# Performance work log

Hardware: AMD Instinct MI355X
Metric: run time of the kernel (lower is better)

Reference implementation:

```python
import jax, jax.numpy as jnp
import numpy as np

# dims
L, E, D, DFF, H = 4, 4, 512, 2048, 8
B, T, S, K = 16, 256, 512, 2
HD = D // H


def _ln(x, g, b, eps=1e-5):
    m = x.mean(-1, keepdims=True)
    v = ((x - m) ** 2).mean(-1, keepdims=True)
    return (x - m) / jnp.sqrt(v + eps) * g + b


def _mha(xq, xkv, in_w, in_b, out_w, out_b):
    # torch nn.MultiheadAttention (batch_first), no masks, eval mode
    qw, kw, vw = jnp.split(in_w, 3, axis=0)
    qb, kb, vb = jnp.split(in_b, 3)
    q = xq @ qw.T + qb                       # [B,T,D]
    k = xkv @ kw.T + kb                      # [B,S,D]
    v = xkv @ vw.T + vb
    def heads(t):
        b, s, _ = t.shape
        return t.reshape(b, s, H, HD).transpose(0, 2, 1, 3)
    q, k, v = heads(q), heads(k), heads(v)   # [B,H,*,HD]
    scale = 1.0 / float(np.sqrt(HD))
    a = jax.nn.softmax(jnp.einsum('bhtd,bhsd->bhts', q, k) * scale, axis=-1)
    o = jnp.einsum('bhts,bhsd->bhtd', a, v)
    o = o.transpose(0, 2, 1, 3).reshape(xq.shape[0], xq.shape[1], D)
    return o @ out_w.T + out_b


def _expert(p, x, mem):
    (siw, sib, sow, sob, ciw, cib, cow, cob,
     l1w, l1b, l2w, l2b, g1, b1, g2, b2, g3, b3) = p
    sa = _mha(x, x, siw, sib, sow, sob)
    x = _ln(x + sa, g1, b1)
    ca = _mha(x, mem, ciw, cib, cow, cob)
    x = _ln(x + ca, g2, b2)
    ffn = jax.nn.relu(x @ l1w.T + l1b) @ l2w.T + l2b
    x = _ln(x + ffn, g3, b3)
    return x


def _forward(tgt, memory, router_w, params):
    x = tgt
    for l in range(L):
        pooled = x.mean(axis=1)                      # [B,D] sample-level routing
        logits = pooled @ router_w[l].T              # [B,E]
        vals, idx = jax.lax.top_k(logits, K)
        w = jax.nn.softmax(vals.astype(jnp.float32), axis=-1).astype(x.dtype)
        # dense [B,E] combine weights: zero for unselected experts -> same math
        wf = jnp.zeros((x.shape[0], E), x.dtype).at[jnp.arange(x.shape[0])[:, None], idx].add(w)
        p_l = jax.tree_util.tree_map(lambda a: a[l], params)   # each [E,...]
        outs = jax.vmap(_expert, in_axes=(0, None, None))(p_l, x, memory)  # [E,B,T,D]
        x = jnp.einsum('be,ebtd->btd', wf, outs)
    return x


def setup_inputs() -> dict:
    key = jax.random.key(0)
    ks = jax.random.split(key, 16)
    n = lambda k, shape: jax.random.normal(k, shape, jnp.float32) * 0.02
    return {
        'tgt': jax.random.normal(ks[0], (B, T, D), jnp.float32),
        'memory': jax.random.normal(ks[1], (B, S, D), jnp.float32),
        'router_w': n(ks[2], (L, E, D)),
        'sa_in_w': n(ks[3], (L, E, 3 * D, D)), 'sa_in_b': jnp.zeros((L, E, 3 * D)),
        'sa_out_w': n(ks[4], (L, E, D, D)), 'sa_out_b': jnp.zeros((L, E, D)),
        'ca_in_w': n(ks[5], (L, E, 3 * D, D)), 'ca_in_b': jnp.zeros((L, E, 3 * D)),
        'ca_out_w': n(ks[6], (L, E, D, D)), 'ca_out_b': jnp.zeros((L, E, D)),
        'lin1_w': n(ks[7], (L, E, DFF, D)), 'lin1_b': jnp.zeros((L, E, DFF)),
        'lin2_w': n(ks[8], (L, E, D, DFF)), 'lin2_b': jnp.zeros((L, E, D)),
        'n1_g': jnp.ones((L, E, D)), 'n1_b': jnp.zeros((L, E, D)),
        'n2_g': jnp.ones((L, E, D)), 'n2_b': jnp.zeros((L, E, D)),
        'n3_g': jnp.ones((L, E, D)), 'n3_b': jnp.zeros((L, E, D)),
    }


def reference(tgt, memory, router_w, sa_in_w, sa_in_b, sa_out_w, sa_out_b,
              ca_in_w, ca_in_b, ca_out_w, ca_out_b, lin1_w, lin1_b, lin2_w, lin2_b,
              n1_g, n1_b, n2_g, n2_b, n3_g, n3_b):
    params = (sa_in_w, sa_in_b, sa_out_w, sa_out_b, ca_in_w, ca_in_b, ca_out_w, ca_out_b,
              lin1_w, lin1_b, lin2_w, lin2_b, n1_g, n1_b, n2_g, n2_b, n3_g, n3_b)
    return _forward(tgt, memory, router_w, params)
```

## Files before the change

kernel.cpp:

```cpp
#include <hip/hip_runtime.h>
#include <hip/hip_bf16.h>

#define L_ 4
#define E_ 4
#define D_ 512
#define DFF_ 2048
#define H_ 8
#define B_ 16
#define T_ 256
#define S_ 512
#define HD_ 64
#define NSLOT 32

typedef __attribute__((ext_vector_type(4))) float f32x4;
typedef __attribute__((ext_vector_type(8))) short bf16x8;
typedef __attribute__((ext_vector_type(4))) int i32x4;

static __device__ __forceinline__ float bf2f(unsigned short u){
  union{float f; unsigned u;} c; c.u = ((unsigned)u)<<16; return c.f;
}
static __device__ __forceinline__ unsigned short f2bf(float f){
  union{float f; unsigned u;} c; c.f=f;
  unsigned u=c.u;
  return (unsigned short)((u + 0x7FFFu + ((u>>16)&1u))>>16);
}

static __device__ __forceinline__ void gload16(const unsigned short* g, unsigned short* l){
  __builtin_amdgcn_global_load_lds(
      (const __attribute__((address_space(1))) void*)g,
      (__attribute__((address_space(3))) void*)l, 16, 0, 0);
}

static __device__ __forceinline__ int xcd_swz(int orig, int nwg){
  int q = nwg >> 3, r = nwg & 7;
  int xcd = orig & 7, idx = orig >> 3;
  return (xcd < r) ? (xcd*(q+1) + idx) : (r*(q+1) + (xcd-r)*q + idx);
}

__global__ void __launch_bounds__(256) pool_k(const float* __restrict__ x,
    float* __restrict__ part)
{
  int b = blockIdx.x >> 3, ch = blockIdx.x & 7;
  int tid = threadIdx.x;
  const float* xp = x + ((long)b*T_ + ch*32)*D_ + tid*2;
  float s0=0.f, s1=0.f;
  #pragma unroll 8
  for (int t=0;t<32;t++){
    float2 v = *(const float2*)(xp + (long)t*D_);
    s0 += v.x; s1 += v.y;
  }
  float* pp = part + ((long)b*8 + ch)*D_ + tid*2;
  pp[0]=s0; pp[1]=s1;
}

__global__ void __launch_bounds__(256) route2_k(const float* __restrict__ part,
    const float* __restrict__ rw, int* __restrict__ eidx, float* __restrict__ wgt)
{
  __shared__ float pooled[D_];
  __shared__ float logit[E_];
  int b = blockIdx.x, tid = threadIdx.x;
  for (int d = tid; d < D_; d += 256){
    float s = 0.f;
    #pragma unroll
    for (int c=0;c<8;c++) s += part[((long)b*8 + c)*D_ + d];
    pooled[d] = s * (1.f/T_);
  }
  __syncthreads();
  int wave = tid>>6, lane = tid&63;
  {
    float s=0.f;
    const float* w = rw + (long)wave*D_;
    for (int d=lane; d<D_; d+=64) s += pooled[d]*w[d];
    #pragma unroll
    for (int o=32;o;o>>=1) s += __shfl_xor(s,o);
    if (lane==0) logit[wave] = s;
  }
  __syncthreads();
  if (tid==0){
    int i1=0; float v1=logit[0];
    for (int e=1;e<E_;e++) if (logit[e] > v1){ v1=logit[e]; i1=e; }
    int i2=-1; float v2=-3.4e38f;
    for (int e=0;e<E_;e++) if (e!=i1 && logit[e] > v2){ v2=logit[e]; i2=e; }
    float e2 = __expf(v2 - v1);
    float w1 = 1.f/(1.f+e2);
    eidx[2*b]=i1; eidx[2*b+1]=i2;
    wgt[2*b]=w1; wgt[2*b+1]=e2*w1;
  }
}

__global__ void __launch_bounds__(256) cast_bf16_k(const float* __restrict__ in,
    unsigned short* __restrict__ out, long n){
  long i = ((long)blockIdx.x*blockDim.x + threadIdx.x)*4;
  long st = (long)gridDim.x*blockDim.x*4;
  for (; i<n; i+=st){
    float4 v = *(const float4*)(in+i);
    ushort4 o; o.x=f2bf(v.x); o.y=f2bf(v.y); o.z=f2bf(v.z); o.w=f2bf(v.w);
    *(ushort4*)(out+i) = o;
  }
}

__global__ void __launch_bounds__(256) cast_weights_k(
    const float* __restrict__ s0, const float* __restrict__ s1,
    const float* __restrict__ s2, const float* __restrict__ s3,
    const float* __restrict__ s4, const float* __restrict__ s5,
    unsigned short* __restrict__ d0, unsigned short* __restrict__ d1,
    unsigned short* __restrict__ d2, unsigned short* __restrict__ d3,
    unsigned short* __restrict__ d4, unsigned short* __restrict__ d5)
{
  const long N0=(long)E_*3*D_*D_, N1=(long)E_*D_*D_;
  const long N2=N0, N3=N1, N4=(long)E_*DFF_*D_, N5=N4;
  const long total = N0+N1+N2+N3+N4+N5;
  long i = ((long)blockIdx.x*256 + threadIdx.x)*4;
  long st = (long)gridDim.x*256*4;
  for (; i<total; i+=st){
    const float* s; unsigned short* d; long j = i;
    if (j < N0){ s=s0; d=d0; }
    else if ((j-=N0) < N1){ s=s1; d=d1; }
    else if ((j-=N1) < N2){ s=s2; d=d2; }
    else if ((j-=N2) < N3){ s=s3; d=d3; }
    else if ((j-=N3) < N4){ s=s4; d=d4; }
    else { j-=N4; s=s5; d=d5; }
    float4 v = *(const float4*)(s+j);
    ushort4 o; o.x=f2bf(v.x); o.y=f2bf(v.y); o.z=f2bf(v.z); o.w=f2bf(v.w);
    *(ushort4*)(d+j) = o;
  }
}

__global__ void __launch_bounds__(256) vtrans_k(const unsigned short* __restrict__ src,
    long sSlot, int ld, unsigned short* __restrict__ dst, int rows)
{
  __shared__ unsigned short t[64][68];
  int s0 = blockIdx.x*64; int h = blockIdx.y; int slot = blockIdx.z;
  const unsigned short* sp = src + (long)slot*sSlot + (long)h*64;
  int c = threadIdx.x&63, w = threadIdx.x>>6;
  #pragma unroll
  for (int i=0;i<16;i++){
    int r = i*4 + w;
    t[r][c] = sp[(long)(s0+r)*ld + c];
  }
  __syncthreads();
  unsigned short* dp = dst + ((long)slot*H_ + h)*((long)64*rows) + s0;
  #pragma unroll
  for (int i=0;i<16;i++){
    int d = i*4 + w;
    dp[(long)d*rows + c] = t[c][d];
  }
}

template<int NT>
__global__ void __launch_bounds__(512) fattn_k(
    const unsigned short* __restrict__ Qg, long qSlot, int ldq,
    const unsigned short* __restrict__ Kg, long kSlot, int ldk,
    const unsigned short* __restrict__ Vtg,
    unsigned short* __restrict__ Og, long oSlot, int ldo)
{
  constexpr int SLEN = NT*64;
  __shared__ unsigned short K_lds[64][72];
  __shared__ unsigned short V_lds[64][72];
  __shared__ unsigned short P_lds[8][16][72];

  int nwg = gridDim.x*gridDim.y;
  int wg = xcd_swz(blockIdx.x + gridDim.x*blockIdx.y, nwg);
  int qb = wg % gridDim.x;
  int z  = wg / gridDim.x;
  int slot = z >> 3, h = z & 7;
  int tid = threadIdx.x, wave = tid>>6, lane = tid&63;
  int lr = lane&15, lg = lane>>4;
  int lk = lg*8;

  const unsigned short* Qp = Qg + (long)slot*qSlot + (long)h*HD_;
  const unsigned short* Kp = Kg + (long)slot*kSlot + (long)h*HD_;
  const unsigned short* Vp = Vtg + (long)z*((long)HD_*SLEN);

  bf16x8 qf[2];
  {
    int qrow = qb*128 + wave*16 + lr;
    const unsigned short* qr = Qp + (long)qrow*ldq;
    qf[0] = *(const bf16x8*)(qr + lk);
    qf[1] = *(const bf16x8*)(qr + 32 + lk);
  }

  float m_prev[4], l_run[4];
  f32x4 acc_o[4];
  #pragma unroll
  for (int r=0;r<4;r++){ m_prev[r]=-1e30f; l_run[r]=0.f; }
  #pragma unroll
  for (int ni=0;ni<4;ni++) acc_o[ni]=(f32x4){0.f,0.f,0.f,0.f};

  int srow = tid>>3, sch = tid&7;

  i32x4 kr0 = *(const i32x4*)(Kp + (long)srow*ldk + sch*8);
  i32x4 vr0 = *(const i32x4*)(Vp + (long)srow*SLEN + sch*8);

  for (int t=0; t<NT; ++t){
    __syncthreads();
    *(i32x4*)&K_lds[srow][sch*8] = kr0;
    *(i32x4*)&V_lds[srow][sch*8] = vr0;
    __syncthreads();

    int tn = (t+1 < NT) ? t+1 : t;
    int k0n = tn*64;
    kr0 = *(const i32x4*)(Kp + (long)(k0n+srow)*ldk + sch*8);
    vr0 = *(const i32x4*)(Vp + (long)srow*SLEN + k0n + sch*8);

    f32x4 s[4];
    #pragma unroll
    for (int ni=0;ni<4;ni++) s[ni]=(f32x4){0.f,0.f,0.f,0.f};
    __builtin_amdgcn_s_setprio(1);
    #pragma unroll
    for (int ki=0;ki<2;ki++){
      #pragma unroll
      for (int ni=0;ni<4;ni++){
        bf16x8 kf = *(const bf16x8*)&K_lds[ni*16+lr][ki*32+lk];
        s[ni] = __builtin_amdgcn_mfma_f32_16x16x32_bf16(qf[ki], kf, s[ni],0,0,0);
      }
    }
    __builtin_amdgcn_s_setprio(0);
    float tmax[4];
    #pragma unroll
    for (int r=0;r<4;r++){
      tmax[r] = fmaxf(fmaxf(s[0][r],s[1][r]),fmaxf(s[2][r],s[3][r]));
      #pragma unroll
      for (int msk=1; msk<16; msk<<=1) tmax[r]=fmaxf(tmax[r], __shfl_xor(tmax[r],msk));
    }
    bool inc = (tmax[0]>m_prev[0])|(tmax[1]>m_prev[1])|(tmax[2]>m_prev[2])|(tmax[3]>m_prev[3]);
    if (__any(inc)){
      #pragma unroll
      for (int r=0;r<4;r++){
        float mnew = fmaxf(m_prev[r], tmax[r]);
        float corr = __expf(m_prev[r]-mnew);
        m_prev[r] = mnew;
        l_run[r] *= corr;
        #pragma unroll
        for (int ni=0;ni<4;ni++) acc_o[ni][r] *= corr;
      }
    }
    float rs[4] = {0.f,0.f,0.f,0.f};
    #pragma unroll
    for (int ni=0;ni<4;ni++){
      #pragma unroll
      for (int r=0;r<4;r++){
        float p = __expf(s[ni][r]-m_prev[r]);
        rs[r] += p;
        P_lds[wave][lg*4+r][ni*16+lr] = f2bf(p);
      }
    }
    #pragma unroll
    for (int r=0;r<4;r++){
      #pragma unroll
      for (int msk=1; msk<16; msk<<=1) rs[r] += __shfl_xor(rs[r],msk);
      l_run[r] += rs[r];
    }
    __builtin_amdgcn_s_setprio(1);
    #pragma unroll
    for (int ki=0;ki<2;ki++){
      bf16x8 pf = *(const bf16x8*)&P_lds[wave][lr][ki*32+lk];
      #pragma unroll
      for (int ni=0;ni<4;ni++){
        bf16x8 vf = *(const bf16x8*)&V_lds[ni*16+lr][ki*32+lk];
        acc_o[ni] = __builtin_amdgcn_mfma_f32_16x16x32_bf16(pf, vf, acc_o[ni],0,0,0);
      }
    }
    __builtin_amdgcn_s_setprio(0);
  }
  unsigned short* Op = Og + (long)slot*oSlot + (long)h*HD_;
  #pragma unroll
  for (int r=0;r<4;r++){
    float inv = 1.f/l_run[r];
    int q = qb*128 + wave*16 + lg*4 + r;
    #pragma unroll
    for (int ni=0;ni<4;ni++)
      Op[(long)q*ldo + ni*16 + lr] = f2bf(acc_o[ni][r]*inv);
  }
}

template<int BM, int BN, int WTM, int WTN, int BK>
__global__ void __launch_bounds__(512) gemm_lds(
    const unsigned short* __restrict__ A, long aSlot, int aDiv, long aHead, int lda,
    const unsigned short* __restrict__ W, long wSlot, long wHead, long wExp, int ldw,
    const int* __restrict__ eidx, const float* __restrict__ bias, long biasExp,
    void* __restrict__ Cp, long cSlot, long cHead, int ldc,
    int K, int HZ, int f32out, int relu, int scaleNlim, float scaleVal)
{
  constexpr int WAVES_N = BN/WTN;
  constexpr int MI = WTM/16, NI = WTN/16;
  constexpr int SLOTS = BK/8;
  static_assert((BM/WTM)*(BN/WTN) == 8, "8 waves");
  static_assert((BM*SLOTS)%512==0 && (BN*SLOTS)%512==0, "stage coverage");
  __shared__ unsigned short smem[2*(BM+BN)*BK];

  int nwg = gridDim.x*gridDim.y*gridDim.z;
  int wg = xcd_swz(blockIdx.x + gridDim.x*(blockIdx.y + gridDim.y*blockIdx.z), nwg);
  int bx = wg % gridDim.x; int t1 = wg / gridDim.x;
  int by = t1 % gridDim.y; int z  = t1 / gridDim.y;

  int slot = z / HZ;
  int h = z - slot*HZ;
  int e = eidx ? eidx[slot] : 0;
  const unsigned short* Ap = A + (long)(slot/aDiv)*aSlot + (long)h*aHead;
  const unsigned short* Wp = W + (long)slot*wSlot + (long)h*wHead + (long)e*wExp;
  const float* bp = bias ? (bias + (long)e*biasExp) : nullptr;

  int tid  = threadIdx.x;
  int wave = tid>>6, lane = tid&63;
  int wm = wave / WAVES_N, wn = wave % WAVES_N;
  int bm0 = by*BM;
  int bn0 = bx*BN;
  int lr = lane&15;
  int lg = lane>>4;
  int swz = (BK==64) ? (lr&7) : ((lr>>1)&3);

  Ap += (long)bm0*lda;
  Wp += (long)bn0*ldw;

  f32x4 acc[MI][NI];
  #pragma unroll
  for (int i=0;i<MI;i++)
  #pragma unroll
  for (int j=0;j<NI;j++) acc[i][j] = (f32x4){0.f,0.f,0.f,0.f};

  auto stage = [&](int buf, int k0){
    unsigned short* as = &smem[(size_t)buf*(BM+BN)*BK];
    unsigned short* bs = as + BM*BK;
    #pragma unroll
    for (int i=0;i<BM*SLOTS/512;i++){
      int cch = i*512 + tid;
      int row = cch / SLOTS, c = cch % SLOTS;
      int cs = (BK==64) ? (c ^ (row&7)) : (c ^ ((row>>1)&3));
      gload16(Ap + (long)row*lda + k0 + (cs<<3), as + cch*8);
    }
    #pragma unroll
    for (int i=0;i<BN*SLOTS/512;i++){
      int cch = i*512 + tid;
      int row = cch / SLOTS, c = cch % SLOTS;
      int cs = (BK==64) ? (c ^ (row&7)) : (c ^ ((row>>1)&3));
      gload16(Wp + (long)row*ldw + k0 + (cs<<3), bs + cch*8);
    }
  };

  auto compute = [&](int buf){
    unsigned short* as = &smem[(size_t)buf*(BM+BN)*BK];
    unsigned short* bs = as + BM*BK;
    #pragma unroll
    for (int ki=0;ki<BK/32;ki++){
      bf16x8 af[MI], bfr[NI];
      #pragma unroll
      for (int mi=0;mi<MI;mi++){
        int row = wm*WTM + mi*16 + lr;
        af[mi] = *(const bf16x8*)&as[row*BK + (((ki*4+lg) ^ swz)<<3)];
      }
      #pragma unroll
      for (int ni=0;ni<NI;ni++){
        int row = wn*WTN + ni*16 + lr;
        bfr[ni] = *(const bf16x8*)&bs[row*BK + (((ki*4+lg) ^ swz)<<3)];
      }
      __builtin_amdgcn_s_setprio(1);
      #pragma unroll
      for (int mi=0;mi<MI;mi++)
      #pragma unroll
      for (int ni=0;ni<NI;ni++)
        acc[mi][ni] = __builtin_amdgcn_mfma_f32_16x16x32_bf16(af[mi], bfr[ni], acc[mi][ni], 0,0,0);
      __builtin_amdgcn_s_setprio(0);
    }
  };

  int NT = K / BK;
  stage(0, 0);
  __syncthreads();
  int cur = 0;
  for (int t=0; t<NT; ++t){
    if (t+1 < NT) stage(cur^1, (t+1)*BK);
    compute(cur);
    __syncthreads();
    cur ^= 1;
  }

  long cbase = (long)slot*cSlot + (long)h*cHead;
  int rbase = lg*4;
  #pragma unroll
  for (int mi=0;mi<MI;mi++)
  #pragma unroll
  for (int ni=0;ni<NI;ni++){
    f32x4 v = acc[mi][ni];
    int n = bn0 + wn*WTN + ni*16 + lr;
    float bv = bp ? bp[n] : 0.f;
    float scv = (n < scaleNlim) ? scaleVal : 1.f;
    #pragma unroll
    for (int r=0;r<4;r++){
      int m = bm0 + wm*WTM + mi*16 + rbase + r;
      float val = (v[r] + bv) * scv;
      if (relu) val = fmaxf(val, 0.f);
      long o = cbase + (long)m*ldc + n;
      if (f32out) ((float*)Cp)[o] = val;
      else ((unsigned short*)Cp)[o] = f2bf(val);
    }
  }
}

template<int ABF>
__global__ void __launch_bounds__(256) add_ln_k(
    const void* __restrict__ Ab_, int aDiv, long aStride,
    const unsigned short* __restrict__ Bb, long bStride,
    const float* __restrict__ G, const float* __restrict__ Bt,
    const int* __restrict__ eidx,
    unsigned short* __restrict__ OutB)
{
  int row = blockIdx.x*4 + (threadIdx.x>>6);
  int slot = row>>8, t = row&255;
  int lane = threadIdx.x&63;
  int d0 = lane*8;
  float x[8];
  if (ABF){
    const unsigned short* a = (const unsigned short*)Ab_ + (long)(slot/aDiv)*aStride + (long)t*D_ + d0;
    ushort4 a0 = *(const ushort4*)a, a1 = *(const ushort4*)(a+4);
    x[0]=bf2f(a0.x); x[1]=bf2f(a0.y); x[2]=bf2f(a0.z); x[3]=bf2f(a0.w);
    x[4]=bf2f(a1.x); x[5]=bf2f(a1.y); x[6]=bf2f(a1.z); x[7]=bf2f(a1.w);
  } else {
    const float* a = (const float*)Ab_ + (long)(slot/aDiv)*aStride + (long)t*D_ + d0;
    float4 a0 = *(const float4*)a, a1 = *(const float4*)(a+4);
    x[0]=a0.x; x[1]=a0.y; x[2]=a0.z; x[3]=a0.w;
    x[4]=a1.x; x[5]=a1.y; x[6]=a1.z; x[7]=a1.w;
  }
  const unsigned short* b = Bb + (long)slot*bStride + (long)t*D_ + d0;
  ushort4 b0 = *(const ushort4*)b, b1 = *(const ushort4*)(b+4);
  x[0]+=bf2f(b0.x); x[1]+=bf2f(b0.y); x[2]+=bf2f(b0.z); x[3]+=bf2f(b0.w);
  x[4]+=bf2f(b1.x); x[5]+=bf2f(b1.y); x[6]+=bf2f(b1.z); x[7]+=bf2f(b1.w);
  float s=0.f;
  #pragma unroll
  for (int i=0;i<8;i++) s += x[i];
  #pragma unroll
  for (int o=32;o;o>>=1) s += __shfl_xor(s,o);
  float m = s*(1.f/D_);
  float q=0.f;
  #pragma unroll
  for (int i=0;i<8;i++){ float d=x[i]-m; q+=d*d; }
  #pragma unroll
  for (int o=32;o;o>>=1) q += __shfl_xor(q,o);
  float rs = rsqrtf(q*(1.f/D_)+1e-5f);
  int e = eidx[slot];
  const float* g  = G  + (long)e*D_ + d0;
  const float* bt = Bt + (long)e*D_ + d0;
  float4 g0 = *(const float4*)g, g1 = *(const float4*)(g+4);
  float4 t0 = *(const float4*)bt, t1 = *(const float4*)(bt+4);
  float gg[8] = {g0.x,g0.y,g0.z,g0.w,g1.x,g1.y,g1.z,g1.w};
  float tt[8] = {t0.x,t0.y,t0.z,t0.w,t1.x,t1.y,t1.z,t1.w};
  long ob = (long)slot*(T_*D_) + (long)t*D_ + d0;
  ushort4 o0, o1;
  float y0=(x[0]-m)*rs*gg[0]+tt[0], y1=(x[1]-m)*rs*gg[1]+tt[1];
  float y2=(x[2]-m)*rs*gg[2]+tt[2], y3=(x[3]-m)*rs*gg[3]+tt[3];
  float y4=(x[4]-m)*rs*gg[4]+tt[4], y5=(x[5]-m)*rs*gg[5]+tt[5];
  float y6=(x[6]-m)*rs*gg[6]+tt[6], y7=(x[7]-m)*rs*gg[7]+tt[7];
  o0.x=f2bf(y0); o0.y=f2bf(y1); o0.z=f2bf(y2); o0.w=f2bf(y3);
  o1.x=f2bf(y4); o1.y=f2bf(y5); o1.z=f2bf(y6); o1.w=f2bf(y7);
  *(ushort4*)(OutB+ob) = o0;
  *(ushort4*)(OutB+ob+4) = o1;
}

__global__ void __launch_bounds__(256) add_ln_comb_k(
    const unsigned short* __restrict__ x2b, const unsigned short* __restrict__ proj,
    const float* __restrict__ G, const float* __restrict__ Bt,
    const int* __restrict__ eidx, const float* __restrict__ wgt,
    float* __restrict__ dstF, unsigned short* __restrict__ dstB)
{
  int row = blockIdx.x*4 + (threadIdx.x>>6);
  int b = row>>8, t = row&255;
  int lane = threadIdx.x&63;
  int d0 = lane*8;
  float out[8];
  #pragma unroll
  for (int i=0;i<8;i++) out[i]=0.f;
  #pragma unroll
  for (int s2i=0;s2i<2;s2i++){
    int slot = 2*b + s2i;
    int e = eidx[slot];
    float w = wgt[slot];
    const unsigned short* a = x2b + (long)slot*(T_*D_) + (long)t*D_ + d0;
    const unsigned short* p = proj + (long)slot*(T_*D_) + (long)t*D_ + d0;
    ushort4 a0 = *(const ushort4*)a, a1 = *(const ushort4*)(a+4);
    ushort4 p0 = *(const ushort4*)p, p1 = *(const ushort4*)(p+4);
    float x[8];
    x[0]=bf2f(a0.x)+bf2f(p0.x); x[1]=bf2f(a0.y)+bf2f(p0.y);
    x[2]=bf2f(a0.z)+bf2f(p0.z); x[3]=bf2f(a0.w)+bf2f(p0.w);
    x[4]=bf2f(a1.x)+bf2f(p1.x); x[5]=bf2f(a1.y)+bf2f(p1.y);
    x[6]=bf2f(a1.z)+bf2f(p1.z); x[7]=bf2f(a1.w)+bf2f(p1.w);
    float s=0.f;
    #pragma unroll
    for (int i=0;i<8;i++) s += x[i];
    #pragma unroll
    for (int o=32;o;o>>=1) s += __shfl_xor(s,o);
    float m = s*(1.f/D_);
    float q=0.f;
    #pragma unroll
    for (int i=0;i<8;i++){ float d=x[i]-m; q+=d*d; }
    #pragma unroll
    for (int o=32;o;o>>=1) q += __shfl_xor(q,o);
    float rs = rsqrtf(q*(1.f/D_)+1e-5f);
    const float* g  = G  + (long)e*D_ + d0;
    const float* bt = Bt + (long)e*D_ + d0;
    float4 g0 = *(const float4*)g, g1 = *(const float4*)(g+4);
    float4 t0 = *(const float4*)bt, t1 = *(const float4*)(bt+4);
    float gg[8] = {g0.x,g0.y,g0.z,g0.w,g1.x,g1.y,g1.z,g1.w};
    float tt[8] = {t0.x,t0.y,t0.z,t0.w,t1.x,t1.y,t1.z,t1.w};
    #pragma unroll
    for (int i=0;i<8;i++) out[i] += w*((x[i]-m)*rs*gg[i]+tt[i]);
  }
  long ob = (long)row*D_ + d0;
  float4 f0 = {out[0],out[1],out[2],out[3]};
  float4 f1 = {out[4],out[5],out[6],out[7]};
  *(float4*)(dstF+ob) = f0;
  *(float4*)(dstF+ob+4) = f1;
  ushort4 o0, o1;
  o0.x=f2bf(out[0]); o0.y=f2bf(out[1]); o0.z=f2bf(out[2]); o0.w=f2bf(out[3]);
  o1.x=f2bf(out[4]); o1.y=f2bf(out[5]); o1.z=f2bf(out[6]); o1.w=f2bf(out[7]);
  *(ushort4*)(dstB+ob) = o0;
  *(ushort4*)(dstB+ob+4) = o1;
}

extern "C" void kernel_launch(void* const* d_in, const int* in_sizes, int n_in,
                              void* d_out, int out_size, void* d_ws, size_t ws_size,
                              hipStream_t stream)
{
  const float* tgt      = (const float*)d_in[0];
  const float* memory   = (const float*)d_in[1];
  const float* router_w = (const float*)d_in[2];
  const float* sa_in_w  = (const float*)d_in[3];
  const float* sa_in_b  = (const float*)d_in[4];
  const float* sa_out_w = (const float*)d_in[5];
  const float* sa_out_b = (const float*)d_in[6];
  const float* ca_in_w  = (const float*)d_in[7];
  const float* ca_in_b  = (const float*)d_in[8];
  const float* ca_out_w = (const float*)d_in[9];
  const float* ca_out_b = (const float*)d_in[10];
  const float* lin1_w   = (const float*)d_in[11];
  const float* lin1_b   = (const float*)d_in[12];
  const float* lin2_w   = (const float*)d_in[13];
  const float* lin2_b   = (const float*)d_in[14];
  const float* n1_g = (const float*)d_in[15];
  const float* n1_b = (const float*)d_in[16];
  const float* n2_g = (const float*)d_in[17];
  const float* n2_b = (const float*)d_in[18];
  const float* n3_g = (const float*)d_in[19];
  const float* n3_b = (const float*)d_in[20];

  char* ws = (char*)d_ws;
  size_t off = 0;
  auto alloc = [&](size_t bytes)->char*{
    char* p = ws + off; off += (bytes + 255) & ~(size_t)255; return p;
  };
  unsigned short* xb    = (unsigned short*)alloc(2ull*B_*T_*D_);
  unsigned short* memb  = (unsigned short*)alloc(2ull*B_*S_*D_);
  float*          x     = (float*)alloc(4ull*B_*T_*D_);
  float*          part  = (float*)alloc(4ull*B_*8*D_);
  int*            eidx  = (int*)alloc(4ull*NSLOT);
  float*          wgt   = (float*)alloc(4ull*NSLOT);
  unsigned short* wSaIn  = (unsigned short*)alloc(2ull*E_*3*D_*D_);
  unsigned short* wSaOut = (unsigned short*)alloc(2ull*E_*D_*D_);
  unsigned short* wCaIn  = (unsigned short*)alloc(2ull*E_*3*D_*D_);
  unsigned short* wCaOut = (unsigned short*)alloc(2ull*E_*D_*D_);
  unsigned short* wL1    = (unsigned short*)alloc(2ull*E_*DFF_*D_);
  unsigned short* wL2    = (unsigned short*)alloc(2ull*E_*D_*DFF_);
  unsigned short* qkv   = (unsigned short*)alloc(2ull*NSLOT*T_*3*D_);
  unsigned short* ffh   = (unsigned short*)alloc(2ull*NSLOT*T_*DFF_);
  unsigned short* attn  = (unsigned short*)alloc(2ull*NSLOT*T_*D_);
  unsigned short* proj  = (unsigned short*)alloc(2ull*NSLOT*T_*D_);
  unsigned short* x1b   = (unsigned short*)alloc(2ull*NSLOT*T_*D_);
  unsigned short* cq    = (unsigned short*)alloc(2ull*NSLOT*T_*D_);
  unsigned short* mkv   = (unsigned short*)alloc(2ull*NSLOT*S_*2*D_);
  unsigned short* x2b   = (unsigned short*)alloc(2ull*NSLOT*T_*D_);
  unsigned short* Vt1   = cq;
  unsigned short* Vt2   = qkv;

  cast_bf16_k<<<1024,256,0,stream>>>(tgt,    xb,   (long)B_*T_*D_);
  cast_bf16_k<<<1024,256,0,stream>>>(memory, memb, (long)B_*S_*D_);

  const float* xcur = tgt;
  for (int l=0; l<L_; ++l){
    pool_k<<<B_*8,256,0,stream>>>(xcur, part);
    route2_k<<<B_,256,0,stream>>>(part, router_w + (size_t)l*E_*D_, eidx, wgt);
    cast_weights_k<<<2048,256,0,stream>>>(
      sa_in_w  + (size_t)l*E_*3*D_*D_, sa_out_w + (size_t)l*E_*D_*D_,
      ca_in_w  + (size_t)l*E_*3*D_*D_, ca_out_w + (size_t)l*E_*D_*D_,
      lin1_w   + (size_t)l*E_*DFF_*D_, lin2_w   + (size_t)l*E_*D_*DFF_,
      wSaIn, wSaOut, wCaIn, wCaOut, wL1, wL2);

    gemm_lds<128,256,64,64,32><<<dim3(6,2,NSLOT),512,0,stream>>>(
      xb, (long)T_*D_, 2, 0, D_,
      wSaIn, 0, 0, (long)3*D_*D_, D_,
      eidx, sa_in_b + (size_t)l*E_*3*D_, 3*D_,
      qkv, (long)T_*3*D_, 0, 3*D_,
      512, 1, 0, 0, D_, 0.125f);
    vtrans_k<<<dim3(T_/64,H_,NSLOT),256,0,stream>>>(
      qkv + 2*D_, (long)T_*3*D_, 3*D_, Vt1, T_);
    fattn_k<4><<<dim3(T_/128, NSLOT*H_),512,0,stream>>>(
      qkv, (long)T_*3*D_, 3*D_,
      qkv + D_, (long)T_*3*D_, 3*D_,
      Vt1, attn, (long)T_*D_, D_);
    gemm_lds<64,128,32,32,64><<<dim3(4,4,NSLOT),512,0,stream>>>(
      attn, (long)T_*D_, 1, 0, D_,
      wSaOut, 0, 0, (long)D_*D_, D_,
      eidx, sa_out_b + (size_t)l*E_*D_, D_,
      proj, (long)T_*D_, 0, D_,
      512, 1, 0, 0, 0, 1.f);
    add_ln_k<0><<<2048,256,0,stream>>>(xcur, 2, (long)T_*D_, proj, (long)T_*D_,
      n1_g + (size_t)l*E_*D_, n1_b + (size_t)l*E_*D_, eidx, x1b);
    gemm_lds<64,128,32,32,64><<<dim3(4,4,NSLOT),512,0,stream>>>(
      x1b, (long)T_*D_, 1, 0, D_,
      wCaIn, 0, 0, (long)3*D_*D_, D_,
      eidx, ca_in_b + (size_t)l*E_*3*D_, 3*D_,
      cq, (long)T_*D_, 0, D_,
      512, 1, 0, 0, D_, 0.125f);
    gemm_lds<128,256,64,64,32><<<dim3(4,4,NSLOT),512,0,stream>>>(
      memb, (long)S_*D_, 2, 0, D_,
      wCaIn + (size_t)D_*D_, 0, 0, (long)3*D_*D_, D_,
      eidx, ca_in_b + (size_t)l*E_*3*D_ + D_, 3*D_,
      mkv, (long)S_*2*D_, 0, 2*D_,
      512, 1, 0, 0, 0, 1.f);
    vtrans_k<<<dim3(S_/64,H_,NSLOT),256,0,stream>>>(
      mkv + D_, (long)S_*2*D_, 2*D_, Vt2, S_);
    fattn_k<8><<<dim3(T_/128, NSLOT*H_),512,0,stream>>>(
      cq, (long)T_*D_, D_,
      mkv, (long)S_*2*D_, 2*D_,
      Vt2, attn, (long)T_*D_, D_);
    gemm_lds<64,128,32,32,64><<<dim3(4,4,NSLOT),512,0,stream>>>(
      attn, (long)T_*D_, 1, 0, D_,
      wCaOut, 0, 0, (long)D_*D_, D_,
      eidx, ca_out_b + (size_t)l*E_*D_, D_,
      proj, (long)T_*D_, 0, D_,
      512, 1, 0, 0, 0, 1.f);
    add_ln_k<1><<<2048,256,0,stream>>>(x1b, 1, (long)T_*D_, proj, (long)T_*D_,
      n2_g + (size_t)l*E_*D_, n2_b + (size_t)l*E_*D_, eidx, x2b);
    gemm_lds<128,256,64,64,32><<<dim3(8,2,NSLOT),512,0,stream>>>(
      x2b, (long)T_*D_, 1, 0, D_,
      wL1, 0, 0, (long)DFF_*D_, D_,
      eidx, lin1_b + (size_t)l*E_*DFF_, DFF_,
      ffh, (long)T_*DFF_, 0, DFF_,
      512, 1, 0, 1, 0, 1.f);
    gemm_lds<64,128,32,32,64><<<dim3(4,4,NSLOT),512,0,stream>>>(
      ffh, (long)T_*DFF_, 1, 0, DFF_,
      wL2, 0, 0, (long)D_*DFF_, DFF_,
      eidx, lin2_b + (size_t)l*E_*D_, D_,
      proj, (long)T_*D_, 0, D_,
      2048, 1, 0, 0, 0, 1.f);
    float* dstF = (l==L_-1) ? (float*)d_out : x;
    add_ln_comb_k<<<1024,256,0,stream>>>(x2b, proj,
      n3_g + (size_t)l*E_*D_, n3_b + (size_t)l*E_*D_, eidx, wgt, dstF, xb);
    xcur = x;
  }
}
```

Measured before the change: 951.2 us.

## Merge self-attn QKV and memory KV projections into one dual GEMM launch

Moves the cross-attention memory K/V projection, which depends only on memory and routing, ahead of self-attention and fuses it with the self-attention QKV projection into a single grouped GEMM launch. The two V-transpose kernels are likewise merged into one launch, which needs a separate Vt2 buffer so the memory V transpose no longer aliases qkv. The aim is fewer kernel launches and larger grids that fill the GPU better. The cost is an extra buffer allocation and more branching in the merged kernels.

```diff
diff --git a/kernel.cpp b/kernel.cpp
--- a/kernel.cpp
+++ b/kernel.cpp
@@ -126,11 +126,18 @@
   }
 }
 
-__global__ void __launch_bounds__(256) vtrans_k(const unsigned short* __restrict__ src,
-    long sSlot, int ld, unsigned short* __restrict__ dst, int rows)
+__global__ void __launch_bounds__(256) vtrans2_k(
+    const unsigned short* __restrict__ src0, long sSlot0, int ld0,
+    unsigned short* __restrict__ dst0, int rows0,
+    const unsigned short* __restrict__ src1, long sSlot1, int ld1,
+    unsigned short* __restrict__ dst1, int rows1)
 {
   __shared__ unsigned short t[64][68];
-  int s0 = blockIdx.x*64; int h = blockIdx.y; int slot = blockIdx.z;
+  int xb = blockIdx.x;
+  const unsigned short* src; long sSlot; int ld; unsigned short* dst; int rows; int s0;
+  if (xb < rows0/64){ src=src0; sSlot=sSlot0; ld=ld0; dst=dst0; rows=rows0; s0=xb*64; }
+  else              { src=src1; sSlot=sSlot1; ld=ld1; dst=dst1; rows=rows1; s0=(xb-rows0/64)*64; }
+  int h = blockIdx.y; int slot = blockIdx.z;
   const unsigned short* sp = src + (long)slot*sSlot + (long)h*64;
   int c = threadIdx.x&63, w = threadIdx.x>>6;
   #pragma unroll
@@ -275,43 +282,24 @@
 }
 
 template<int BM, int BN, int WTM, int WTN, int BK>
-__global__ void __launch_bounds__(512) gemm_lds(
-    const unsigned short* __restrict__ A, long aSlot, int aDiv, long aHead, int lda,
-    const unsigned short* __restrict__ W, long wSlot, long wHead, long wExp, int ldw,
-    const int* __restrict__ eidx, const float* __restrict__ bias, long biasExp,
-    void* __restrict__ Cp, long cSlot, long cHead, int ldc,
-    int K, int HZ, int f32out, int relu, int scaleNlim, float scaleVal)
+static __device__ __forceinline__ void gemm_core(
+    const unsigned short* __restrict__ Ap,
+    const unsigned short* __restrict__ Wp,
+    const float* __restrict__ bp,
+    void* __restrict__ Cp, long cbase, int ldc,
+    int lda, int ldw, int bm0, int bn0,
+    int K, int f32out, int relu, int scaleNlim, float scaleVal,
+    unsigned short* smem)
 {
   constexpr int WAVES_N = BN/WTN;
   constexpr int MI = WTM/16, NI = WTN/16;
   constexpr int SLOTS = BK/8;
-  static_assert((BM/WTM)*(BN/WTN) == 8, "8 waves");
-  static_assert((BM*SLOTS)%512==0 && (BN*SLOTS)%512==0, "stage coverage");
-  __shared__ unsigned short smem[2*(BM+BN)*BK];
-
-  int nwg = gridDim.x*gridDim.y*gridDim.z;
-  int wg = xcd_swz(blockIdx.x + gridDim.x*(blockIdx.y + gridDim.y*blockIdx.z), nwg);
-  int bx = wg % gridDim.x; int t1 = wg / gridDim.x;
-  int by = t1 % gridDim.y; int z  = t1 / gridDim.y;
-
-  int slot = z / HZ;
-  int h = z - slot*HZ;
-  int e = eidx ? eidx[slot] : 0;
-  const unsigned short* Ap = A + (long)(slot/aDiv)*aSlot + (long)h*aHead;
-  const unsigned short* Wp = W + (long)slot*wSlot + (long)h*wHead + (long)e*wExp;
-  const float* bp = bias ? (bias + (long)e*biasExp) : nullptr;
-
   int tid  = threadIdx.x;
   int wave = tid>>6, lane = tid&63;
   int wm = wave / WAVES_N, wn = wave % WAVES_N;
-  int bm0 = by*BM;
-  int bn0 = bx*BN;
   int lr = lane&15;
   int lg = lane>>4;
   int swz = (BK==64) ? (lr&7) : ((lr>>1)&3);
-
-  Ap += (long)bm0*lda;
-  Wp += (long)bn0*ldw;
 
   f32x4 acc[MI][NI];
   #pragma unroll
@@ -375,7 +363,6 @@
     cur ^= 1;
   }
 
-  long cbase = (long)slot*cSlot + (long)h*cHead;
   int rbase = lg*4;
   #pragma unroll
   for (int mi=0;mi<MI;mi++)
@@ -395,6 +382,77 @@
       else ((unsigned short*)Cp)[o] = f2bf(val);
     }
   }
+}
+
+template<int BM, int BN, int WTM, int WTN, int BK>
+__global__ void __launch_bounds__(512) gemm_lds(
+    const unsigned short* __restrict__ A, long aSlot, int aDiv, long aHead, int lda,
+    const unsigned short* __restrict__ W, long wSlot, long wHead, long wExp, int ldw,
+    const int* __restrict__ eidx, const float* __restrict__ bias, long biasExp,
+    void* __restrict__ Cp, long cSlot, long cHead, int ldc,
+    int K, int HZ, int f32out, int relu, int scaleNlim, float scaleVal)
+{
+  constexpr int SLOTS = BK/8;
+  static_assert((BM/WTM)*(BN/WTN) == 8, "8 waves");
+  static_assert((BM*SLOTS)%512==0 && (BN*SLOTS)%512==0, "stage coverage");
+  __shared__ unsigned short smem[2*(BM+BN)*BK];
+
+  int nwg = gridDim.x*gridDim.y*gridDim.z;
+  int wg = xcd_swz(blockIdx.x + gridDim.x*(blockIdx.y + gridDim.y*blockIdx.z), nwg);
+  int bx = wg % gridDim.x; int t1 = wg / gridDim.x;
+  int by = t1 % gridDim.y; int z  = t1 / gridDim.y;
+
+  int slot = z / HZ;
+  int h = z - slot*HZ;
+  int e = eidx ? eidx[slot] : 0;
+  const unsigned short* Ap = A + (long)(slot/aDiv)*aSlot + (long)h*aHead + (long)by*BM*lda;
+  const unsigned short* Wp = W + (long)slot*wSlot + (long)h*wHead + (long)e*wExp + (long)bx*BN*ldw;
+  const float* bp = bias ? (bias + (long)e*biasExp) : nullptr;
+  long cbase = (long)slot*cSlot + (long)h*cHead;
+
+  gemm_core<BM,BN,WTM,WTN,BK>(Ap, Wp, bp, Cp, cbase, ldc, lda, ldw,
+      by*BM, bx*BN, K, f32out, relu, scaleNlim, scaleVal, smem);
+}
+
+__global__ void __launch_bounds__(512) gemm_dual(
+    const unsigned short* __restrict__ A0, long aSlot0,
+    const unsigned short* __restrict__ W0, const float* __restrict__ bias0,
+    unsigned short* __restrict__ C0, long cSlot0, int ldc0,
+    const unsigned short* __restrict__ A1, long aSlot1,
+    const unsigned short* __restrict__ W1, const float* __restrict__ bias1,
+    unsigned short* __restrict__ C1, long cSlot1, int ldc1,
+    const int* __restrict__ eidx)
+{
+  constexpr int BM=128, BN=256, WTM=64, WTN=64, BK=32;
+  __shared__ unsigned short smem[2*(BM+BN)*BK];
+  const int NBLK0 = 6*2*NSLOT;
+  int nwg = gridDim.x;
+  int wg = xcd_swz(blockIdx.x, nwg);
+
+  const unsigned short *Ap, *Wp; const float* bp;
+  unsigned short* Cp; long cbase; int ldc, bm0, bn0, scaleNlim;
+  if (wg < NBLK0){
+    int bx = wg % 6; int t1 = wg / 6;
+    int by = t1 % 2; int slot = t1 / 2;
+    int e = eidx[slot];
+    bm0 = by*BM; bn0 = bx*BN;
+    Ap = A0 + (long)(slot/2)*aSlot0 + (long)bm0*D_;
+    Wp = W0 + (long)e*(3*D_*D_) + (long)bn0*D_;
+    bp = bias0 + (long)e*(3*D_);
+    Cp = C0; cbase = (long)slot*cSlot0; ldc = ldc0; scaleNlim = D_;
+  } else {
+    int w1 = wg - NBLK0;
+    int bx = w1 % 4; int t1 = w1 / 4;
+    int by = t1 % 4; int slot = t1 / 4;
+    int e = eidx[slot];
+    bm0 = by*BM; bn0 = bx*BN;
+    Ap = A1 + (long)(slot/2)*aSlot1 + (long)bm0*D_;
+    Wp = W1 + (long)e*(3*D_*D_) + (long)bn0*D_;
+    bp = bias1 + (long)e*(3*D_);
+    Cp = C1; cbase = (long)slot*cSlot1; ldc = ldc1; scaleNlim = 0;
+  }
+  gemm_core<BM,BN,WTM,WTN,BK>(Ap, Wp, bp, Cp, cbase, ldc, D_, D_,
+      bm0, bn0, 512, 0, 0, scaleNlim, 0.125f, smem);
 }
 
 template<int ABF>
@@ -567,8 +625,8 @@
   unsigned short* cq    = (unsigned short*)alloc(2ull*NSLOT*T_*D_);
   unsigned short* mkv   = (unsigned short*)alloc(2ull*NSLOT*S_*2*D_);
   unsigned short* x2b   = (unsigned short*)alloc(2ull*NSLOT*T_*D_);
+  unsigned short* Vt2   = (unsigned short*)alloc(2ull*NSLOT*H_*HD_*S_);
   unsigned short* Vt1   = cq;
-  unsigned short* Vt2   = qkv;
 
   cast_bf16_k<<<1024,256,0,stream>>>(tgt,    xb,   (long)B_*T_*D_);
   cast_bf16_k<<<1024,256,0,stream>>>(memory, memb, (long)B_*S_*D_);
@@ -583,14 +641,15 @@
       lin1_w   + (size_t)l*E_*DFF_*D_, lin2_w   + (size_t)l*E_*D_*DFF_,
       wSaIn, wSaOut, wCaIn, wCaOut, wL1, wL2);
 
-    gemm_lds<128,256,64,64,32><<<dim3(6,2,NSLOT),512,0,stream>>>(
-      xb, (long)T_*D_, 2, 0, D_,
-      wSaIn, 0, 0, (long)3*D_*D_, D_,
-      eidx, sa_in_b + (size_t)l*E_*3*D_, 3*D_,
-      qkv, (long)T_*3*D_, 0, 3*D_,
-      512, 1, 0, 0, D_, 0.125f);
-    vtrans_k<<<dim3(T_/64,H_,NSLOT),256,0,stream>>>(
-      qkv + 2*D_, (long)T_*3*D_, 3*D_, Vt1, T_);
+    gemm_dual<<<dim3(6*2*NSLOT + 4*4*NSLOT),512,0,stream>>>(
+      xb,   (long)T_*D_, wSaIn,                sa_in_b + (size_t)l*E_*3*D_,
+      qkv,  (long)T_*3*D_, 3*D_,
+      memb, (long)S_*D_, wCaIn + (size_t)D_*D_, ca_in_b + (size_t)l*E_*3*D_ + D_,
+      mkv,  (long)S_*2*D_, 2*D_,
+      eidx);
+    vtrans2_k<<<dim3(T_/64 + S_/64, H_, NSLOT),256,0,stream>>>(
+      qkv + 2*D_, (long)T_*3*D_, 3*D_, Vt1, T_,
+      mkv + D_,   (long)S_*2*D_, 2*D_, Vt2, S_);
     fattn_k<4><<<dim3(T_/128, NSLOT*H_),512,0,stream>>>(
       qkv, (long)T_*3*D_, 3*D_,
       qkv + D_, (long)T_*3*D_, 3*D_,
@@ -609,14 +668,6 @@
       eidx, ca_in_b + (size_t)l*E_*3*D_, 3*D_,
       cq, (long)T_*D_, 0, D_,
       512, 1, 0, 0, D_, 0.125f);
-    gemm_lds<128,256,64,64,32><<<dim3(4,4,NSLOT),512,0,stream>>>(
-      memb, (long)S_*D_, 2, 0, D_,
-      wCaIn + (size_t)D_*D_, 0, 0, (long)3*D_*D_, D_,
-      eidx, ca_in_b + (size_t)l*E_*3*D_ + D_, 3*D_,
-      mkv, (long)S_*2*D_, 0, 2*D_,
-      512, 1, 0, 0, 0, 1.f);
-    vtrans_k<<<dim3(S_/64,H_,NSLOT),256,0,stream>>>(
-      mkv + D_, (long)S_*2*D_, 2*D_, Vt2, S_);
     fattn_k<8><<<dim3(T_/128, NSLOT*H_),512,0,stream>>>(
       cq, (long)T_*D_, D_,
       mkv, (long)S_*2*D_, 2*D_,
```

Result: no change. 934.0 us (-1.8%).
